# Kernel tuning notes

Measured on AMD Instinct MI355X. Metric: run time of the kernel, lower is better.

## Reference

```python
import jax, jax.numpy as jnp
import numpy as np

N_USER = 100000
N_ITEM = 50000
N_NODES = N_USER + N_ITEM
NNZ = 4800000
EMB = 64
N_LAYERS = 3
BATCH = 16384
EPS = 1e-12
NEG_SLOPE = 0.2


def setup_inputs() -> dict:
    key = jax.random.key(0)
    ks = jax.random.split(key, 12)
    # symmetric-normalized adjacency values ~ 1/degree scale
    adj_vals = jax.random.uniform(ks[0], (NNZ,), dtype=jnp.float32) / 32.0
    return {
        "user_idx": jax.random.randint(ks[1], (BATCH,), 0, N_USER, dtype=jnp.int32),
        "item_idx": jax.random.randint(ks[2], (BATCH,), 0, N_ITEM, dtype=jnp.int32),
        "adj_rows": jax.random.randint(ks[3], (NNZ,), 0, N_NODES, dtype=jnp.int32),
        "adj_cols": jax.random.randint(ks[4], (NNZ,), 0, N_NODES, dtype=jnp.int32),
        "adj_vals": adj_vals,
        "user_emb": jax.random.normal(ks[5], (N_USER, EMB), dtype=jnp.float32) * 0.1,
        "item_emb": jax.random.normal(ks[6], (N_ITEM, EMB), dtype=jnp.float32) * 0.1,
        "W_gc": jax.random.normal(ks[7], (N_LAYERS, EMB, EMB), dtype=jnp.float32) * 0.1,
        "b_gc": jax.random.normal(ks[8], (N_LAYERS, 1, EMB), dtype=jnp.float32) * 0.1,
        "W_bi": jax.random.normal(ks[9], (N_LAYERS, EMB, EMB), dtype=jnp.float32) * 0.1,
        "b_bi": jax.random.normal(ks[10], (N_LAYERS, 1, EMB), dtype=jnp.float32) * 0.1,
        "W_out": jax.random.normal(ks[11], (4 * EMB, 1), dtype=jnp.float32) * 0.1,
        "b_out": jnp.zeros((1,), dtype=jnp.float32),
    }


def _ngcf_embeddings(adj_rows, adj_cols, adj_vals, user_emb, item_emb,
                     W_gc, b_gc, W_bi, b_bi):
    ego = jnp.concatenate([user_emb, item_emb], axis=0)  # [N, 64]
    all_embs = [ego]
    for k in range(N_LAYERS):
        # sparse A_hat @ ego: gather source rows, weight, scatter-add to dest rows
        msgs = adj_vals[:, None] * ego[adj_cols]                 # [nnz, 64]
        side = jax.ops.segment_sum(msgs, adj_rows, num_segments=N_NODES)
        sum_emb = side @ W_gc[k] + b_gc[k]
        bi_emb = (ego * side) @ W_bi[k] + b_bi[k]
        ego = jax.nn.leaky_relu(sum_emb + bi_emb, negative_slope=NEG_SLOPE)
        # mess_dropout = 0 (eval), then L2-normalize rows (F.normalize semantics)
        nrm = jnp.linalg.norm(ego, axis=1, keepdims=True)
        all_embs.append(ego / jnp.maximum(nrm, EPS))
    return jnp.concatenate(all_embs, axis=1)  # [N, 256]


def reference(user_idx, item_idx, adj_rows, adj_cols, adj_vals,
              user_emb, item_emb, W_gc, b_gc, W_bi, b_bi, W_out, b_out):
    all_emb = _ngcf_embeddings(adj_rows, adj_cols, adj_vals, user_emb, item_emb,
                               W_gc, b_gc, W_bi, b_bi)
    u = all_emb[user_idx]                 # [B, 256]
    i = all_emb[N_USER + item_idx]        # [B, 256]
    logits = (u * i) @ W_out + b_out      # GMF head
    return jax.nn.sigmoid(logits)         # [B, 1]
```

## Files before the change

### kernel.cpp

```cpp
#include <hip/hip_runtime.h>

#define N_USER  100000
#define N_ITEM  50000
#define N_NODES 150000
#define NNZ     4800000
#define EMB     64
#define BATCH   16384
#define NEG_SLOPE 0.2f

#define NB_C   512
#define NPB    ((N_NODES + NB_C - 1) / NB_C)
#define CHUNK  8192
#define NCH    ((NNZ + CHUNK - 1) / CHUNK)

#define WFRAG_ELEMS (3 * 2 * 2 * 4 * 64 * 8)

typedef unsigned int  uint;
typedef unsigned short u16;
typedef short bf16x8 __attribute__((ext_vector_type(8)));
typedef float f32x4  __attribute__((ext_vector_type(4)));

static __device__ __forceinline__ u16 f2bf(float f) {
    uint u = __float_as_uint(f);
    return (u16)((u + 0x7fffu + ((u >> 16) & 1u)) >> 16);
}
static __device__ __forceinline__ float bf2f(u16 h) {
    return __uint_as_float((uint)h << 16);
}

__global__ void ngcf_concat(const float4* __restrict__ ue,
                            const float4* __restrict__ ie,
                            ushort4* __restrict__ ego) {
    const int n4_user  = N_USER * EMB / 4;
    const int n4_total = N_NODES * EMB / 4;
    int i = blockIdx.x * blockDim.x + threadIdx.x;
    if (i >= n4_total) return;
    float4 v = (i < n4_user) ? ue[i] : ie[i - n4_user];
    ushort4 o;
    o.x = f2bf(v.x); o.y = f2bf(v.y); o.z = f2bf(v.z); o.w = f2bf(v.w);
    ego[i] = o;
}

__global__ void ngcf_prep(const float* __restrict__ Wgc,
                          const float* __restrict__ Wbi,
                          const float* __restrict__ bgc,
                          const float* __restrict__ bbi,
                          u16* __restrict__ wfrag, float* __restrict__ bias) {
    int t = blockIdx.x * blockDim.x + threadIdx.x;
    if (t < WFRAG_ELEMS) {
        int i     = t & 7;
        int lane  = (t >> 3) & 63;
        int w     = (t >> 9) & 3;
        int ks    = (t >> 11) & 1;
        int mat   = (t >> 12) & 1;
        int layer = t >> 13;
        int k = ks * 32 + (lane >> 4) * 8 + i;
        int n = w * 16 + (lane & 15);
        const float* W = mat ? Wbi : Wgc;
        wfrag[t] = f2bf(W[(layer * 64 + k) * 64 + n]);
    }
    int u = t - WFRAG_ELEMS;
    if (u >= 0 && u < 3 * 64)
        bias[u] = bgc[u] + bbi[u];
}

__global__ void ngcf_coarse_hist(const int* __restrict__ rows,
                                 int* __restrict__ ccnt) {
    __shared__ int bins[NB_C];
    bins[threadIdx.x] = 0;
    bins[threadIdx.x + 256] = 0;
    __syncthreads();
    int stride = gridDim.x * blockDim.x;
    for (int e = blockIdx.x * blockDim.x + threadIdx.x; e < NNZ; e += stride)
        atomicAdd(&bins[rows[e] / NPB], 1);
    __syncthreads();
    int v0 = bins[threadIdx.x], v1 = bins[threadIdx.x + 256];
    if (v0) atomicAdd(&ccnt[threadIdx.x], v0);
    if (v1) atomicAdd(&ccnt[threadIdx.x + 256], v1);
}

__global__ void ngcf_coarse_scan(const int* __restrict__ ccnt,
                                 int* __restrict__ coffs,
                                 int* __restrict__ gcursor) {
    __shared__ int wsum[8];
    int t = threadIdx.x, lane = t & 63, wv = t >> 6;
    int v = ccnt[t];
    int inc = v;
    #pragma unroll
    for (int off = 1; off < 64; off <<= 1) {
        int u = __shfl_up(inc, off);
        if (lane >= off) inc += u;
    }
    if (lane == 63) wsum[wv] = inc;
    __syncthreads();
    int base = 0;
    #pragma unroll
    for (int w = 0; w < 8; ++w) base += (w < wv) ? wsum[w] : 0;
    int incl = base + inc;
    int excl = incl - v;
    coffs[t]   = excl;
    gcursor[t] = excl;
    if (t == NB_C - 1) coffs[NB_C] = incl;
}

__global__ __launch_bounds__(512) void ngcf_coarse_scatter(
        const int* __restrict__ rows, const int* __restrict__ cols,
        const float* __restrict__ vals,
        int* __restrict__ gcursor,
        int2* __restrict__ tmp_cv, u16* __restrict__ tmp_lr) {
    __shared__ int bins[NB_C];
    __shared__ int rbase[NB_C];
    const int t = threadIdx.x;
    const int e0 = blockIdx.x * CHUNK;
    bins[t] = 0;
    __syncthreads();
    #pragma unroll
    for (int i = 0; i < CHUNK / 512; ++i) {
        int e = e0 + i * 512 + t;
        if (e < NNZ) atomicAdd(&bins[rows[e] / NPB], 1);
    }
    __syncthreads();
    int c = bins[t];
    if (c > 0) rbase[t] = atomicAdd(&gcursor[t], c);
    bins[t] = 0;
    __syncthreads();
    #pragma unroll
    for (int i = 0; i < CHUNK / 512; ++i) {
        int e = e0 + i * 512 + t;
        if (e < NNZ) {
            int r  = rows[e];
            int b  = r / NPB;
            int lr = r - b * NPB;
            int rk = atomicAdd(&bins[b], 1);
            int pos = rbase[b] + rk;
            int2 E; E.x = cols[e]; E.y = __float_as_int(vals[e]);
            tmp_cv[pos] = E;
            tmp_lr[pos] = (u16)lr;
        }
    }
}

__global__ __launch_bounds__(512) void ngcf_fine_sort(
        const int* __restrict__ coffs,
        const int2* __restrict__ tmp_cv, const u16* __restrict__ tmp_lr,
        int* __restrict__ offs, int2* __restrict__ edges) {
    __shared__ int s[512];
    const int b   = blockIdx.x;
    const int t   = threadIdx.x;
    const int nlo = b * NPB;
    const int nhi = min(nlo + NPB, N_NODES);
    const int nn  = nhi - nlo;
    const int clo = coffs[b];
    const int chi = coffs[b + 1];

    s[t] = 0;
    __syncthreads();
    for (int e = clo + t; e < chi; e += 512)
        atomicAdd(&s[tmp_lr[e]], 1);
    __syncthreads();
    int v = s[t];
    for (int d = 1; d < 512; d <<= 1) {
        int u = (t >= d) ? s[t - d] : 0;
        __syncthreads();
        s[t] += u;
        __syncthreads();
    }
    int excl = s[t] - v;
    if (t < nn) offs[nlo + t] = clo + excl;
    __syncthreads();
    s[t] = clo + excl;
    __syncthreads();
    for (int e = clo + t; e < chi; e += 512) {
        int lr = tmp_lr[e];
        int p  = atomicAdd(&s[lr], 1);
        edges[p] = tmp_cv[e];
    }
    if (b == NB_C - 1 && t == 0) offs[N_NODES] = chi;
}

__global__ __launch_bounds__(256) void ngcf_spmm_mfma(
        const u16* __restrict__ src, u16* __restrict__ dst,
        const int* __restrict__ offs, const int2* __restrict__ edges,
        const u16* __restrict__ wfrag, const float* __restrict__ bias,
        int layer) {
    __shared__ float sideL[16][68];
    __shared__ float biL[16][68];

    const int wave = threadIdx.x >> 6;
    const int lane = threadIdx.x & 63;
    const int g    = lane >> 4;
    const int q    = lane & 15;
    const int node = blockIdx.x * 16 + wave * 4 + g;

    const int sBeg = offs[node];
    const int deg  = offs[node + 1] - sBeg;

    const long long* ep  = (const long long*)edges;
    const ushort4*   s4p = (const ushort4*)src;

    float a0 = 0.f, a1 = 0.f, a2 = 0.f, a3 = 0.f;
    for (int base = 0; __any(base < deg); base += 16) {
        int idx = base + q;
        long long L = 0;
        if (idx < deg) L = __builtin_nontemporal_load(ep + sBeg + idx);
        int Ec = (int)L;
        int Ev = (int)(L >> 32);
        #pragma unroll
        for (int j = 0; j < 16; ++j) {
            int   c = __shfl(Ec, (g << 4) + j);
            float v = __int_as_float(__shfl(Ev, (g << 4) + j));
            ushort4 s4 = s4p[(size_t)c * 16 + q];
            a0 += v * bf2f(s4.x);
            a1 += v * bf2f(s4.y);
            a2 += v * bf2f(s4.z);
            a3 += v * bf2f(s4.w);
        }
    }

    ushort4 egov = s4p[(size_t)node * 16 + q];
    const int r = wave * 4 + g;
    float4 sv; sv.x = a0; sv.y = a1; sv.z = a2; sv.w = a3;
    float4 bv; bv.x = bf2f(egov.x) * a0; bv.y = bf2f(egov.y) * a1;
    bv.z = bf2f(egov.z) * a2; bv.w = bf2f(egov.w) * a3;
    *(float4*)&sideL[r][4 * q] = sv;
    *(float4*)&biL[r][4 * q]   = bv;
    __syncthreads();

    const int m  = lane & 15;
    const int kh = lane >> 4;
    f32x4 acc = {0.f, 0.f, 0.f, 0.f};
    const bf16x8* wf = (const bf16x8*)wfrag;

    #pragma unroll
    for (int ks = 0; ks < 2; ++ks) {
        const int k0 = ks * 32 + kh * 8;
        bf16x8 As, Ab;
        #pragma unroll
        for (int j = 0; j < 8; ++j) {
            As[j] = (short)f2bf(sideL[m][k0 + j]);
            Ab[j] = (short)f2bf(biL[m][k0 + j]);
        }
        bf16x8 Bg = wf[(((layer * 2 + 0) * 2 + ks) * 4 + wave) * 64 + lane];
        bf16x8 Bb = wf[(((layer * 2 + 1) * 2 + ks) * 4 + wave) * 64 + lane];
        acc = __builtin_amdgcn_mfma_f32_16x16x32_bf16(As, Bg, acc, 0, 0, 0);
        acc = __builtin_amdgcn_mfma_f32_16x16x32_bf16(Ab, Bb, acc, 0, 0, 0);
    }

    const int col = wave * 16 + m;
    const float bs = bias[layer * 64 + col];
    #pragma unroll
    for (int i = 0; i < 4; ++i) {
        int nd = kh * 4 + i;
        float o = acc[i] + bs;
        o = o > 0.f ? o : NEG_SLOPE * o;
        dst[(size_t)(blockIdx.x * 16 + nd) * 64 + col] = f2bf(o);
    }
}

__global__ void ngcf_batch(const int* __restrict__ uidx,
                           const int* __restrict__ iidx,
                           const u16* __restrict__ ego,
                           const float* __restrict__ Wout,
                           float* __restrict__ partial,
                           int layer, int normalize) {
    int b = blockIdx.x * (blockDim.x >> 6) + (threadIdx.x >> 6);
    int lane = threadIdx.x & 63;
    if (b >= BATCH) return;
    int u  = uidx[b];
    int it = N_USER + iidx[b];
    float eu = bf2f(ego[((size_t)u  << 6) + lane]);
    float ei = bf2f(ego[((size_t)it << 6) + lane]);
    float w  = Wout[(layer << 6) + lane];
    float dot = eu * ei * w;
    float nu = eu * eu, ni = ei * ei;
    #pragma unroll
    for (int off = 32; off; off >>= 1) {
        dot += __shfl_xor(dot, off);
        nu  += __shfl_xor(nu,  off);
        ni  += __shfl_xor(ni,  off);
    }
    if (lane == 0) {
        float val;
        if (normalize) {
            float denom = fmaxf(sqrtf(nu), 1e-12f) * fmaxf(sqrtf(ni), 1e-12f);
            val = dot / denom;
        } else {
            val = dot;
        }
        if (layer == 0) partial[b] = val;
        else            partial[b] += val;
    }
}

__global__ void ngcf_final(const float* __restrict__ partial,
                           const float* __restrict__ bout,
                           float* __restrict__ out) {
    int b = blockIdx.x * blockDim.x + threadIdx.x;
    if (b < BATCH) {
        float x = partial[b] + bout[0];
        out[b] = 1.f / (1.f + expf(-x));
    }
}

extern "C" void kernel_launch(void* const* d_in, const int* in_sizes, int n_in,
                              void* d_out, int out_size, void* d_ws, size_t ws_size,
                              hipStream_t stream) {
    const int*   user_idx = (const int*)  d_in[0];
    const int*   item_idx = (const int*)  d_in[1];
    const int*   adj_rows = (const int*)  d_in[2];
    const int*   adj_cols = (const int*)  d_in[3];
    const float* adj_vals = (const float*)d_in[4];
    const float* user_emb = (const float*)d_in[5];
    const float* item_emb = (const float*)d_in[6];
    const float* W_gc     = (const float*)d_in[7];
    const float* b_gc     = (const float*)d_in[8];
    const float* W_bi     = (const float*)d_in[9];
    const float* b_bi     = (const float*)d_in[10];
    const float* W_out    = (const float*)d_in[11];
    const float* b_out    = (const float*)d_in[12];
    float* out = (float*)d_out;

    const size_t NODE_F = (size_t)N_NODES * EMB;

    char* base = (char*)d_ws;
    size_t off = 0;
    auto carve = [&](size_t bytes) {
        char* p = base + off;
        off = (off + bytes + 255) & ~(size_t)255;
        return p;
    };
    u16*   ego0    = (u16*)  carve(NODE_F * 2);
    u16*   ego1    = (u16*)  carve(NODE_F * 2);
    int2*  edges   = (int2*) carve((size_t)NNZ * 8);
    int2*  tmp_cv  = (int2*) carve((size_t)NNZ * 8);
    u16*   tmp_lr  = (u16*)  carve((size_t)NNZ * 2);
    int*   offs    = (int*)  carve((N_NODES + 1) * 4);
    int*   ccnt    = (int*)  carve(NB_C * 4);
    int*   coffs   = (int*)  carve((NB_C + 1) * 4);
    int*   gcursor = (int*)  carve(NB_C * 4);
    u16*   wfrag   = (u16*)  carve(WFRAG_ELEMS * 2);
    float* bias    = (float*)carve(3 * 64 * 4);
    float* partial = (float*)carve(BATCH * 4);
    (void)ws_size;

    ngcf_concat<<<(N_NODES * EMB / 4 + 255) / 256, 256, 0, stream>>>(
        (const float4*)user_emb, (const float4*)item_emb, (ushort4*)ego0);

    ngcf_prep<<<(WFRAG_ELEMS + 3 * 64 + 255) / 256, 256, 0, stream>>>(
        W_gc, W_bi, b_gc, b_bi, wfrag, bias);

    hipMemsetAsync(ccnt, 0, NB_C * sizeof(int), stream);
    ngcf_coarse_hist   <<<1024, 256, 0, stream>>>(adj_rows, ccnt);
    ngcf_coarse_scan   <<<1, NB_C, 0, stream>>>(ccnt, coffs, gcursor);
    ngcf_coarse_scatter<<<NCH, 512, 0, stream>>>(adj_rows, adj_cols, adj_vals,
                                                 gcursor, tmp_cv, tmp_lr);
    ngcf_fine_sort     <<<NB_C, 512, 0, stream>>>(coffs, tmp_cv, tmp_lr,
                                                  offs, edges);

    ngcf_batch<<<BATCH / 4, 256, 0, stream>>>(user_idx, item_idx, ego0,
                                              W_out, partial, 0, 0);

    u16* src = ego0;
    u16* dst = ego1;
    for (int k = 0; k < 3; ++k) {
        ngcf_spmm_mfma<<<N_NODES / 16, 256, 0, stream>>>(
            src, dst, offs, edges, wfrag, bias, k);
        ngcf_batch<<<BATCH / 4, 256, 0, stream>>>(user_idx, item_idx, dst,
                                                  W_out, partial, k + 1, 1);
        u16* t = src; src = dst; dst = t;
    }
    ngcf_final<<<(BATCH + 255) / 256, 256, 0, stream>>>(partial, b_out, out);
}
```

Measured before the change: 696.9 us.

## Stage coarse-scatter bucket output in LDS and pack edges into 64-bit words

The coarse scatter kernel now does a local prefix scan over its bucket counts and writes packed edges into an LDS staging buffer sorted by bucket. It then copies them out in contiguous runs, so global writes become mostly coalesced instead of scattered. Column, value and local row are packed into one 64-bit word (18-bit col, 9-bit local row), which removes the separate u16 array and its extra scattered stores. The chunk size drops so the 48KB staging buffer fits in LDS, at the cost of a binary search per output element and more blocks.

Result: faster. 559.8 us (-19.7%).

```diff
diff --git a/kernel.cpp b/kernel.cpp
--- a/kernel.cpp
+++ b/kernel.cpp
@@ -10,13 +10,14 @@
 
 #define NB_C   512
 #define NPB    ((N_NODES + NB_C - 1) / NB_C)
-#define CHUNK  8192
+#define CHUNK  6144
 #define NCH    ((NNZ + CHUNK - 1) / CHUNK)
 
 #define WFRAG_ELEMS (3 * 2 * 2 * 4 * 64 * 8)
 
 typedef unsigned int  uint;
 typedef unsigned short u16;
+typedef unsigned long long u64;
 typedef short bf16x8 __attribute__((ext_vector_type(8)));
 typedef float f32x4  __attribute__((ext_vector_type(4)));
 
@@ -107,11 +108,17 @@
         const int* __restrict__ rows, const int* __restrict__ cols,
         const float* __restrict__ vals,
         int* __restrict__ gcursor,
-        int2* __restrict__ tmp_cv, u16* __restrict__ tmp_lr) {
+        u64* __restrict__ tmp) {
     __shared__ int bins[NB_C];
-    __shared__ int rbase[NB_C];
-    const int t = threadIdx.x;
+    __shared__ int lbase_s[NB_C + 1];
+    __shared__ int delta_s[NB_C];
+    __shared__ int wsum[8];
+    __shared__ u64 stage[CHUNK];
+
+    const int t  = threadIdx.x;
     const int e0 = blockIdx.x * CHUNK;
+    const int cnt = min(CHUNK, NNZ - e0);
+
     bins[t] = 0;
     __syncthreads();
     #pragma unroll
@@ -120,8 +127,25 @@
         if (e < NNZ) atomicAdd(&bins[rows[e] / NPB], 1);
     }
     __syncthreads();
-    int c = bins[t];
-    if (c > 0) rbase[t] = atomicAdd(&gcursor[t], c);
+    int v = bins[t];
+    int lane = t & 63, wv = t >> 6;
+    int inc = v;
+    #pragma unroll
+    for (int off = 1; off < 64; off <<= 1) {
+        int u = __shfl_up(inc, off);
+        if (lane >= off) inc += u;
+    }
+    if (lane == 63) wsum[wv] = inc;
+    __syncthreads();
+    int base = 0;
+    #pragma unroll
+    for (int w = 0; w < 8; ++w) base += (w < wv) ? wsum[w] : 0;
+    int incl = base + inc;
+    int excl = incl - v;
+    lbase_s[t] = excl;
+    if (t == NB_C - 1) lbase_s[NB_C] = incl;
+    int myrbase = (v > 0) ? atomicAdd(&gcursor[t], v) : 0;
+    delta_s[t] = myrbase - excl;
     bins[t] = 0;
     __syncthreads();
     #pragma unroll
@@ -132,17 +156,26 @@
             int b  = r / NPB;
             int lr = r - b * NPB;
             int rk = atomicAdd(&bins[b], 1);
-            int pos = rbase[b] + rk;
-            int2 E; E.x = cols[e]; E.y = __float_as_int(vals[e]);
-            tmp_cv[pos] = E;
-            tmp_lr[pos] = (u16)lr;
+            u64 P = ((u64)(uint)__float_as_int(vals[e]) << 32)
+                  | ((uint)cols[e] << 9) | (uint)lr;
+            stage[lbase_s[b] + rk] = P;
         }
+    }
+    __syncthreads();
+    for (int i = t; i < cnt; i += 512) {
+        int b = 0;
+        #pragma unroll
+        for (int s = 256; s >= 1; s >>= 1) {
+            int nb = b + s;
+            if (nb <= NB_C - 1 && lbase_s[nb] <= i) b = nb;
+        }
+        tmp[delta_s[b] + i] = stage[i];
     }
 }
 
 __global__ __launch_bounds__(512) void ngcf_fine_sort(
         const int* __restrict__ coffs,
-        const int2* __restrict__ tmp_cv, const u16* __restrict__ tmp_lr,
+        const u64* __restrict__ tmp,
         int* __restrict__ offs, int2* __restrict__ edges) {
     __shared__ int s[512];
     const int b   = blockIdx.x;
@@ -156,7 +189,7 @@
     s[t] = 0;
     __syncthreads();
     for (int e = clo + t; e < chi; e += 512)
-        atomicAdd(&s[tmp_lr[e]], 1);
+        atomicAdd(&s[(int)(tmp[e] & 511u)], 1);
     __syncthreads();
     int v = s[t];
     for (int d = 1; d < 512; d <<= 1) {
@@ -171,9 +204,13 @@
     s[t] = clo + excl;
     __syncthreads();
     for (int e = clo + t; e < chi; e += 512) {
-        int lr = tmp_lr[e];
+        u64 P  = tmp[e];
+        int lr = (int)(P & 511u);
         int p  = atomicAdd(&s[lr], 1);
-        edges[p] = tmp_cv[e];
+        int2 E;
+        E.x = (int)((P >> 9) & 0x3FFFFu);
+        E.y = (int)(P >> 32);
+        edges[p] = E;
     }
     if (b == NB_C - 1 && t == 0) offs[N_NODES] = chi;
 }
@@ -332,8 +369,7 @@
     u16*   ego0    = (u16*)  carve(NODE_F * 2);
     u16*   ego1    = (u16*)  carve(NODE_F * 2);
     int2*  edges   = (int2*) carve((size_t)NNZ * 8);
-    int2*  tmp_cv  = (int2*) carve((size_t)NNZ * 8);
-    u16*   tmp_lr  = (u16*)  carve((size_t)NNZ * 2);
+    u64*   tmp     = (u64*)  carve((size_t)NNZ * 8);
     int*   offs    = (int*)  carve((N_NODES + 1) * 4);
     int*   ccnt    = (int*)  carve(NB_C * 4);
     int*   coffs   = (int*)  carve((NB_C + 1) * 4);
@@ -353,9 +389,8 @@
     ngcf_coarse_hist   <<<1024, 256, 0, stream>>>(adj_rows, ccnt);
     ngcf_coarse_scan   <<<1, NB_C, 0, stream>>>(ccnt, coffs, gcursor);
     ngcf_coarse_scatter<<<NCH, 512, 0, stream>>>(adj_rows, adj_cols, adj_vals,
-                                                 gcursor, tmp_cv, tmp_lr);
-    ngcf_fine_sort     <<<NB_C, 512, 0, stream>>>(coffs, tmp_cv, tmp_lr,
-                                                  offs, edges);
+                                                 gcursor, tmp);
+    ngcf_fine_sort     <<<NB_C, 512, 0, stream>>>(coffs, tmp, offs, edges);
 
     ngcf_batch<<<BATCH / 4, 256, 0, stream>>>(user_idx, item_idx, ego0,
                                               W_out, partial, 0, 0);
```
